# Optimization experiments

Hardware: AMD Instinct MI355X
Metric: run time of the kernel (lower is better)

## Reference

```python
import jax, jax.numpy as jnp
import numpy as np

B_, L_, D_ = 2, 4096, 1024
E_ = 2
DI = E_ * D_            # 2048
H_ = 16
HD_ = DI // H_          # 128
N_ = 128
K_ = 4                  # d_conv
CS_ = 256               # SSD chunk size
MC_ = 256               # Hebbian memory chunk size
ALPHA = 0.5             # memory_alpha (== write_alpha default)


def _silu(x):
    return x * jax.nn.sigmoid(x)


def _rmsnorm(x, w, eps=1e-6):
    return x * jax.lax.rsqrt(jnp.mean(x * x, axis=-1, keepdims=True) + eps) * w


def setup_inputs() -> dict:
    key = jax.random.key(0)
    ks = jax.random.split(key, 8)
    proj_dim = 2 * DI + 2 * H_ * N_ + H_
    n = lambda k, sh, sc: jax.random.normal(k, sh, jnp.float32) * sc
    return {
        "x": n(ks[0], (B_, L_, D_), 1.0),
        "norm_w": jnp.ones((D_,), jnp.float32),
        "w_in": n(ks[1], (proj_dim, D_), 0.02),
        "conv_w": n(ks[2], (DI, K_), 0.2),
        "conv_b": jnp.zeros((DI,), jnp.float32),
        "A_log": jnp.log(2.0 * jnp.ones((H_,), jnp.float32)),
        "dt_bias": jnp.zeros((H_,), jnp.float32),
        "D_skip": jnp.ones((DI,), jnp.float32),
        "w_out": n(ks[3], (D_, DI), 0.02),
        "w_write": n(ks[4], (D_, D_), 0.02),
        "w_read": n(ks[5], (D_, D_), 0.02),
        "decay": jnp.float32(4.6),
    }


def _forward(x, norm_w, w_in, conv_w, conv_b, A_log, dt_bias, D_skip,
             w_out, w_write, w_read, decay):
    B, L, D = x.shape
    residual = x
    xn = _rmsnorm(x, norm_w)

    # ---- SSDBlock ----
    proj = xn @ w_in.T  # (B,L,2*DI+2*H*N+H)
    val = proj[..., :DI]
    gate = proj[..., DI:2 * DI]
    Bp = proj[..., 2 * DI:2 * DI + H_ * N_].reshape(B, L, H_, N_)
    Cp = proj[..., 2 * DI + H_ * N_:2 * DI + 2 * H_ * N_].reshape(B, L, H_, N_)
    dt = jax.nn.softplus(proj[..., -H_:] + dt_bias)  # (B,L,H)

    # causal depthwise conv1d (kernel K_, groups=DI)
    vp = jnp.pad(val, ((0, 0), (K_ - 1, 0), (0, 0)))
    val = sum(conv_w[:, k] * vp[:, k:k + L, :] for k in range(K_)) + conv_b
    val = _silu(val).reshape(B, L, H_, HD_)

    ld = dt * (-jnp.exp(A_log))  # log decay (B,L,H)

    nc = L // CS_
    to_chunks = lambda a: jnp.moveaxis(a.reshape(B, nc, CS_, *a.shape[2:]), 1, 0)
    tril = jnp.tril(jnp.ones((CS_, CS_), bool))
    Dv = D_skip.reshape(1, H_, 1, HD_)

    def ssd_chunk(h, inp):
        v_c, b_c, c_c, ld_c = inp  # (B,CS,H,HD), (B,CS,H,N), (B,CS,H,N), (B,CS,H)
        cum = jnp.cumsum(ld_c, axis=1)            # (B,CS,H)
        cum_h = jnp.transpose(cum, (0, 2, 1))     # (B,H,CS)
        dd = cum_h[:, :, :, None] - cum_h[:, :, None, :]
        Lmat = jnp.where(tril, jnp.exp(dd), 0.0)
        M = jnp.einsum('blhn,bmhn->bhlm', c_c, b_c) * Lmat
        v_h = jnp.transpose(v_c, (0, 2, 1, 3))    # (B,H,CS,HD)
        Y = M @ v_h
        Y = Y + jnp.einsum('blhn,bhdn,blh->bhld', c_c, h, jnp.exp(cum))
        Y = Y + Dv * v_h
        h = jnp.exp(cum[:, -1])[:, :, None, None] * h + \
            jnp.einsum('blhd,blhn,blh->bhdn', v_c, b_c, jnp.exp(cum[:, -1:, :] - cum))
        return h, Y

    h0 = jnp.zeros((B, H_, HD_, N_), jnp.float32)
    _, Ys = jax.lax.scan(ssd_chunk, h0,
                         (to_chunks(val), to_chunks(Bp), to_chunks(Cp), to_chunks(ld)))
    # (nc,B,H,CS,HD) -> (B,L,DI)
    Y = jnp.transpose(Ys, (1, 0, 3, 2, 4)).reshape(B, L, DI)
    out = (Y * _silu(gate)) @ w_out.T  # (B,L,D)

    # ---- Hebbian memory (chunkwise) ----
    gamma = jax.nn.sigmoid(decay)
    lg = jnp.log(gamma)
    v = out @ w_write.T
    wk = jnp.pad(out[:, :-1], ((0, 0), (1, 0), (0, 0)))  # shifted write keys
    p = jnp.arange(MC_)
    diffs = jnp.maximum(p[:, None] - 1 - p[None, :], 0).astype(jnp.float32)
    causal = (p[:, None] > p[None, :]).astype(jnp.float32)
    Mmem = jnp.exp(diffs * lg) * causal
    gp = gamma ** p                    # read decay by position in chunk
    gw = gamma ** (MC_ - 1 - p)        # write decay to end of chunk
    nm = L // MC_
    tom = lambda a: jnp.moveaxis(a.reshape(B, nm, MC_, D), 1, 0)

    def mem_chunk(W, inp):
        rk_c, wk_c, v_c = inp  # (B,MC,D)
        inter = jnp.einsum('bde,bte->btd', W, rk_c) * gp[None, :, None]
        S = jnp.einsum('bie,bje->bij', rk_c, wk_c)
        intra = (S * Mmem) @ v_c
        W = gamma ** MC_ * W + jnp.einsum('btd,bte->bde', v_c * gw[None, :, None], wk_c)
        return W, inter + intra

    W0 = jnp.zeros((B, D, D), jnp.float32)
    _, reads = jax.lax.scan(mem_chunk, W0, (tom(out), tom(wk), tom(v)))
    reads = jnp.moveaxis(reads, 0, 1).reshape(B, L, D)
    out = out + ALPHA * (reads @ w_read.T)
    return residual + out


def reference(x, norm_w, w_in, conv_w, conv_b, A_log, dt_bias, D_skip,
              w_out, w_write, w_read, decay):
    return _forward(x, norm_w, w_in, conv_w, conv_b, A_log, dt_bias, D_skip,
                    w_out, w_write, w_read, decay)
```

## Files before the change

kernel.cpp:

```cpp
#include <hip/hip_runtime.h>
#include <hip/hip_bf16.h>

typedef __hip_bfloat16 bf16;
typedef __attribute__((ext_vector_type(8))) short short8;
typedef __attribute__((ext_vector_type(4))) float floatx4;

#define B_ 2
#define L_ 4096
#define D_ 1024
#define DI_ 2048
#define H_ 16
#define HD_ 128
#define N_ 128
#define CS_ 256
#define MC_ 256
#define NC_ 16
#define PROJ_ 8208

__device__ __forceinline__ float bf2f(short s) {
    return __uint_as_float(((unsigned)(unsigned short)s) << 16);
}

__device__ __forceinline__ void gl_lds16(const void* g, void* s) {
    __builtin_amdgcn_global_load_lds(
        (const __attribute__((address_space(1))) void*)g,
        (__attribute__((address_space(3))) void*)s, 16, 0, 0);
}

struct GemmP {
    const bf16* A; const bf16* Bt;
    float* C; bf16* CB; bf16* CB2; bf16* CB3;
    const float* add0; const float* add1; const bf16* add0b; const float* scr;
    long lda, ldb, ldc;
    int M, N, K, zinner;
    long a_zo, a_zi, b_zo, b_zi, c_zo, c_zi;
};

template<int EPI>
__global__ __launch_bounds__(256, 2) void gemm_bt(GemmP p)
{
    int NT = gridDim.x, MT = gridDim.y;
    long T = (long)NT * MT * gridDim.z;
    long flat = ((long)blockIdx.z * MT + blockIdx.y) * NT + blockIdx.x;
    int xcd = (int)(flat & 7);
    long q = flat >> 3;
    long Tq = T >> 3; int Tr = (int)(T & 7);
    long tile = (long)xcd * Tq + (long)(xcd < Tr ? xcd : Tr) + q;
    long per_z = (long)NT * MT;
    int z = (int)(tile / per_z);
    int t2 = (int)(tile - (long)z * per_z);
    int FG = NT >> 3;
    int g, width, within;
    if (t2 < FG * MT * 8) { g = t2 / (MT * 8); width = 8; within = t2 - g * MT * 8; }
    else                  { g = FG; width = NT - FG * 8; within = t2 - FG * MT * 8; }
    int m_outer = within / (8 * width);
    int hb = MT - m_outer * 8; if (hb > 8) hb = 8;
    int inner = within - m_outer * 8 * width;
    int n_in = inner / hb, m_in = inner - n_in * hb;
    int m0 = (m_outer * 8 + m_in) * 128;
    int n0 = (g * 8 + n_in) * 128;

    int zo = z / p.zinner, zi = z % p.zinner;
    const bf16* A  = p.A  + (long)zo * p.a_zo + (long)zi * p.a_zi;
    const bf16* Bt = p.Bt + (long)zo * p.b_zo + (long)zi * p.b_zi;
    long coff = (long)zo * p.c_zo + (long)zi * p.c_zi;

    __shared__ __align__(16) bf16 As[128 * 64];
    __shared__ __align__(16) bf16 Bs[128 * 64];

    int tid = threadIdx.x;
    int lane = tid & 63, wave = tid >> 6;
    int wm = (wave >> 1) * 64, wn = (wave & 1) * 64;
    int r16 = lane & 15, q8 = (lane >> 4) * 8;

    floatx4 zero4 = {0.f, 0.f, 0.f, 0.f};
    floatx4 acc[4][4];
#pragma unroll
    for (int i = 0; i < 4; i++)
#pragma unroll
        for (int j = 0; j < 4; j++) acc[i][j] = zero4;

    int lrow = lane >> 3;
    int lc = ((lane & 7) ^ lrow) * 8;
    int wrow = wave * 32;
    int rx = lane & 7;

    for (int k0 = 0; k0 < p.K; k0 += 64) {
#pragma unroll
        for (int t = 0; t < 4; t++) {
            int row = wrow + t * 8 + lrow;
            gl_lds16(A + (long)(m0 + row) * p.lda + k0 + lc, &As[(wrow + t * 8) * 64]);
            int bn = n0 + row; if (bn > p.N - 1) bn = p.N - 1;
            gl_lds16(Bt + (long)bn * p.ldb + k0 + lc, &Bs[(wrow + t * 8) * 64]);
        }
        __syncthreads();
#pragma unroll
        for (int ks = 0; ks < 64; ks += 32) {
            int lb = (ks >> 3) + (lane >> 4);
            int po = ((lb ^ rx) << 3);
            short8 af[4], bq[4];
#pragma unroll
            for (int i = 0; i < 4; i++)
                af[i] = *(const short8*)&As[(wm + i * 16 + r16) * 64 + po];
#pragma unroll
            for (int j = 0; j < 4; j++)
                bq[j] = *(const short8*)&Bs[(wn + j * 16 + r16) * 64 + po];
#pragma unroll
            for (int i = 0; i < 4; i++)
#pragma unroll
                for (int j = 0; j < 4; j++)
                    acc[i][j] = __builtin_amdgcn_mfma_f32_16x16x32_bf16(af[i], bq[j], acc[i][j], 0, 0, 0);
        }
        __syncthreads();
    }

    int rq = (lane >> 4) * 4;
#pragma unroll
    for (int i = 0; i < 4; i++) {
#pragma unroll
        for (int j = 0; j < 4; j++) {
#pragma unroll
            for (int r = 0; r < 4; r++) {
                int gm = m0 + wm + i * 16 + rq + r;
                int gn = n0 + wn + j * 16 + r16;
                if (gm >= p.M || gn >= p.N) continue;
                float a = acc[i][j][r];
                if (EPI == 0) {
                    p.C[coff + (long)gm * p.ldc + gn] = a;
                } else if (EPI == 1) {
                    long ix = coff + (long)gm * p.ldc + gn;
                    p.C[ix] = a; p.CB[ix] = __float2bfloat16(a);
                } else if (EPI == 2) {
                    if (gn < 2048)      p.CB [(long)gm * 2048 + gn]          = __float2bfloat16(a);
                    else if (gn < 4096) p.CB2[(long)gm * 2048 + (gn - 2048)] = __float2bfloat16(a);
                    else if (gn < 8192) p.CB3[(long)gm * 4096 + (gn - 4096)] = __float2bfloat16(a);
                    else                p.C  [(long)gm * 16   + (gn - 8192)] = a;
                } else if (EPI == 3) {
                    float lg = p.scr[1];
                    float v = (gm > gn) ? a * __expf((float)(gm - 1 - gn) * lg) : 0.f;
                    p.CB[coff + (long)gm * p.ldc + gn] = __float2bfloat16(v);
                } else if (EPI == 4) {
                    long ix = coff + (long)gm * p.ldc + gn;
                    float t = a * p.scr[16 + gm] + __bfloat162float(p.add0b[ix]);
                    p.CB[ix] = __float2bfloat16(t);
                } else if (EPI == 5) {
                    long ix = (long)gm * p.ldc + gn;
                    p.C[ix] = p.add0[ix] + p.add1[ix] + 0.5f * a;
                } else if (EPI == 6) {
                    p.CB[coff + (long)gm * p.ldc + gn] = __float2bfloat16(a);
                }
            }
        }
    }
}

__global__ void k_gamma(const float* decay, float* scr)
{
    int t = threadIdx.x;
    float g = 1.f / (1.f + expf(-decay[0]));
    float lg = logf(g);
    if (t == 0) { scr[0] = g; scr[1] = lg; scr[2] = expf(256.f * lg); }
    scr[16 + t]  = expf(lg * (float)t);
    scr[272 + t] = expf(lg * (float)(255 - t));
}

__global__ void k_f2b(const float* __restrict__ s, bf16* __restrict__ d, long n4)
{
    long i = (long)blockIdx.x * 256 + threadIdx.x;
    if (i >= n4) return;
    float4 v = ((const float4*)s)[i];
    bf16* o = d + i * 4;
    o[0] = __float2bfloat16(v.x); o[1] = __float2bfloat16(v.y);
    o[2] = __float2bfloat16(v.z); o[3] = __float2bfloat16(v.w);
}

__global__ __launch_bounds__(256) void k_rmsnorm(const float* __restrict__ x,
                                                 const float* __restrict__ w,
                                                 bf16* __restrict__ o)
{
    int row = blockIdx.x, t = threadIdx.x;
    float4 xv = ((const float4*)(x + (long)row * D_))[t];
    float s = xv.x*xv.x + xv.y*xv.y + xv.z*xv.z + xv.w*xv.w;
#pragma unroll
    for (int m = 32; m > 0; m >>= 1) s += __shfl_xor(s, m, 64);
    __shared__ float ps[4];
    if ((t & 63) == 0) ps[t >> 6] = s;
    __syncthreads();
    s = ps[0] + ps[1] + ps[2] + ps[3];
    float r = rsqrtf(s * (1.f / (float)D_) + 1e-6f);
    float4 wv = ((const float4*)w)[t];
    bf16* orow = o + (long)row * D_ + t * 4;
    orow[0] = __float2bfloat16(xv.x * r * wv.x);
    orow[1] = __float2bfloat16(xv.y * r * wv.y);
    orow[2] = __float2bfloat16(xv.z * r * wv.z);
    orow[3] = __float2bfloat16(xv.w * r * wv.w);
}

__global__ void k_ld(const float* __restrict__ dtr, const float* __restrict__ dt_bias,
                     const float* __restrict__ A_log, float* __restrict__ ld)
{
    long i = (long)blockIdx.x * 256 + threadIdx.x;
    if (i >= (long)B_ * L_ * H_) return;
    int h = (int)(i & 15);
    float d = dtr[i] + dt_bias[h];
    float sp = (d > 20.f) ? d : log1pf(__expf(d));
    ld[i] = -__expf(A_log[h]) * sp;
}

__global__ __launch_bounds__(256) void k_cum(const float* __restrict__ ld,
                                             float* __restrict__ cum_g,
                                             float* __restrict__ cumlast)
{
    int bid = blockIdx.x;
    int h = bid & 15, c = (bid >> 4) & 15, b = bid >> 8;
    long rowbase = (long)b * L_ + c * CS_;
    int tid = threadIdx.x;
    __shared__ float cum_s[256];
    cum_s[tid] = ld[(rowbase + tid) * H_ + h];
    __syncthreads();
    for (int off = 1; off < 256; off <<= 1) {
        float add = (tid >= off) ? cum_s[tid - off] : 0.f;
        __syncthreads();
        cum_s[tid] += add;
        __syncthreads();
    }
    cum_g[(rowbase + tid) * H_ + h] = cum_s[tid];
    if (tid == 255) cumlast[bid] = cum_s[255];
}

__global__ void k_conv(const bf16* __restrict__ val_b, const float* __restrict__ cw,
                       const float* __restrict__ cb, bf16* __restrict__ vo)
{
    long idx = (long)blockIdx.x * 256 + threadIdx.x;
    if (idx >= (long)B_ * L_ * DI_) return;
    long row = idx >> 11; int ch = (int)(idx & 2047);
    int l = (int)(row & (L_ - 1));
    float acc = cb[ch];
#pragma unroll
    for (int k = 0; k < 4; k++) {
        int ls = l - 3 + k;
        if (ls >= 0) acc += cw[ch * 4 + k] * __bfloat162float(val_b[(row - 3 + k) * 2048 + ch]);
    }
    float s = acc / (1.f + __expf(-acc));
    vo[idx] = __float2bfloat16(s);
}

__global__ void k_vt(const bf16* __restrict__ vconv, const float* __restrict__ cum_g,
                     const float* __restrict__ cumlast, bf16* __restrict__ vT,
                     bf16* __restrict__ vTw)
{
    __shared__ bf16 tile[32][33];
    int b = blockIdx.z;
    int r0 = blockIdx.x * 32, c0 = blockIdx.y * 32;
    int tx = threadIdx.x & 31, ty = threadIdx.x >> 5;
    for (int i = 0; i < 32; i += 8)
        tile[ty + i][tx] = vconv[((long)b * L_ + r0 + ty + i) * 2048 + c0 + tx];
    __syncthreads();
    int l = r0 + tx;
    int h = c0 >> 7;
    float w = __expf(cumlast[b * 256 + (l >> 8) * 16 + h] - cum_g[((long)b * L_ + l) * 16 + h]);
    for (int i = 0; i < 32; i += 8) {
        int col = c0 + ty + i;
        long oidx = ((long)b * 2048 + col) * L_ + l;
        bf16 v = tile[tx][ty + i];
        vT[oidx] = v;
        vTw[oidx] = __float2bfloat16(__bfloat162float(v) * w);
    }
}

__global__ void k_bt(const bf16* __restrict__ bc, bf16* __restrict__ BT)
{
    __shared__ bf16 tile[32][33];
    int b = blockIdx.z;
    int r0 = blockIdx.x * 32, c0 = blockIdx.y * 32;
    int tx = threadIdx.x & 31, ty = threadIdx.x >> 5;
    for (int i = 0; i < 32; i += 8)
        tile[ty + i][tx] = bc[((long)b * L_ + r0 + ty + i) * 4096 + c0 + tx];
    __syncthreads();
    int l = r0 + tx;
    for (int i = 0; i < 32; i += 8) {
        int col = c0 + ty + i;
        BT[((long)b * 2048 + col) * L_ + l] = tile[tx][ty + i];
    }
}

__global__ __launch_bounds__(256, 2) void k_ssd_u2(
    const bf16* __restrict__ vTw, const bf16* __restrict__ BT, float* __restrict__ U)
{
    int bid = blockIdx.x;
    int h = bid & 15, c = (bid >> 4) & 15, b = bid >> 8;
    int lane = threadIdx.x & 63, wave = threadIdx.x >> 6;
    int r16 = lane & 15, q8 = (lane >> 4) * 8, rq = (lane >> 4) * 4;
    int d0 = (wave >> 1) * 64, n0 = (wave & 1) * 64;
    const bf16* vb = vTw + ((long)b * 2048 + h * 128) * L_ + c * 256;
    const bf16* bb = BT  + ((long)b * 2048 + h * 128) * L_ + c * 256;
    floatx4 zero4 = {0.f, 0.f, 0.f, 0.f};
    floatx4 acc[4][4];
#pragma unroll
    for (int i = 0; i < 4; i++)
#pragma unroll
        for (int j = 0; j < 4; j++) acc[i][j] = zero4;
#pragma unroll 2
    for (int ks = 0; ks < 8; ks++) {
        short8 af[4], bq[4];
#pragma unroll
        for (int i = 0; i < 4; i++)
            af[i] = *(const short8*)(vb + (long)(d0 + i * 16 + r16) * L_ + ks * 32 + q8);
#pragma unroll
        for (int j = 0; j < 4; j++)
            bq[j] = *(const short8*)(bb + (long)(n0 + j * 16 + r16) * L_ + ks * 32 + q8);
#pragma unroll
        for (int i = 0; i < 4; i++)
#pragma unroll
            for (int j = 0; j < 4; j++)
                acc[i][j] = __builtin_amdgcn_mfma_f32_16x16x32_bf16(af[i], bq[j], acc[i][j], 0, 0, 0);
    }
    float* up = U + (((long)c * B_ + b) * H_ + h) * 16384;
#pragma unroll
    for (int i = 0; i < 4; i++)
#pragma unroll
        for (int j = 0; j < 4; j++)
#pragma unroll
            for (int r = 0; r < 4; r++)
                up[(d0 + i * 16 + rq + r) * 128 + (n0 + j * 16 + r16)] = acc[i][j][r];
}

__global__ void k_ssd2(const float* __restrict__ U, const float* __restrict__ cumlast,
                       bf16* __restrict__ hst)
{
    long idx = (long)blockIdx.x * 256 + threadIdx.x;
    const long tot = (long)B_ * H_ * HD_ * N_;
    if (idx >= tot) return;
    int bh = (int)(idx >> 14);
    int b = bh >> 4, h = bh & 15;
    float hv = 0.f;
    for (int c = 0; c < NC_; c++) {
        hst[c * tot + idx] = __float2bfloat16(hv);
        float ef = __expf(cumlast[b * 256 + c * 16 + h]);
        hv = ef * hv + U[c * tot + idx];
    }
}

__global__ __launch_bounds__(256, 2) void k_ssd_y(
    const bf16* __restrict__ bc_b, const bf16* __restrict__ vT,
    const bf16* __restrict__ hst, const float* __restrict__ cum_g,
    const float* __restrict__ Dskip, const bf16* __restrict__ gate_b,
    bf16* __restrict__ yg)
{
    int bid = blockIdx.x;
    int h = bid & 15, c = (bid >> 4) & 15, b = bid >> 8;
    long rowbase = (long)b * L_ + c * CS_;
    int tid = threadIdx.x, lane = tid & 63, wave = tid >> 6;
    int r16 = lane & 15, q8 = (lane >> 4) * 8, rq = (lane >> 4) * 4;
    int wt = (wave >> 1) * 32, wmS = (wave & 1) * 32, wd = (wave & 1) * 64;

    __shared__ float cum_s[256];
    __shared__ __align__(16) bf16 Ss[64][72];

    cum_s[tid] = cum_g[(rowbase + tid) * H_ + h];
    __syncthreads();

    const bf16* Cb  = bc_b + rowbase * 4096 + 2048 + h * 128;
    const bf16* Bb  = bc_b + rowbase * 4096 + h * 128;
    const bf16* vTb = vT + ((long)b * 2048 + h * 128) * L_ + c * 256;
    const bf16* hp  = hst + (((long)c * B_ + b) * H_ + h) * 16384;

    floatx4 zero4 = {0.f, 0.f, 0.f, 0.f};

    for (int tt = 0; tt < 4; tt++) {
        int tbase = tt * 64;
        short8 caf[2][4];
#pragma unroll
        for (int i = 0; i < 2; i++)
#pragma unroll
            for (int ks = 0; ks < 4; ks++)
                caf[i][ks] = *(const short8*)(Cb + (long)(tbase + wt + i * 16 + r16) * 4096 + ks * 32 + q8);

        floatx4 yacc[2][4];
#pragma unroll
        for (int i = 0; i < 2; i++)
#pragma unroll
            for (int j = 0; j < 4; j++) yacc[i][j] = zero4;
#pragma unroll
        for (int ks = 0; ks < 4; ks++)
#pragma unroll
            for (int j = 0; j < 4; j++) {
                short8 hq = *(const short8*)(hp + (long)(wd + j * 16 + r16) * 128 + ks * 32 + q8);
#pragma unroll
                for (int i = 0; i < 2; i++)
                    yacc[i][j] = __builtin_amdgcn_mfma_f32_16x16x32_bf16(caf[i][ks], hq, yacc[i][j], 0, 0, 0);
            }
        float texp[2][4];
#pragma unroll
        for (int i = 0; i < 2; i++)
#pragma unroll
            for (int r = 0; r < 4; r++)
                texp[i][r] = __expf(cum_s[tbase + wt + i * 16 + rq + r]);
#pragma unroll
        for (int i = 0; i < 2; i++)
#pragma unroll
            for (int j = 0; j < 4; j++)
#pragma unroll
                for (int r = 0; r < 4; r++) yacc[i][j][r] *= texp[i][r];

        for (int mt = 0; mt <= tt; mt++) {
            int mbase = mt * 64;
            floatx4 sacc[2][2];
#pragma unroll
            for (int i = 0; i < 2; i++)
#pragma unroll
                for (int j = 0; j < 2; j++) sacc[i][j] = zero4;
#pragma unroll
            for (int ks = 0; ks < 4; ks++) {
                short8 bq[2];
#pragma unroll
                for (int j = 0; j < 2; j++)
                    bq[j] = *(const short8*)(Bb + (long)(mbase + wmS + j * 16 + r16) * 4096 + ks * 32 + q8);
#pragma unroll
                for (int i = 0; i < 2; i++)
#pragma unroll
                    for (int j = 0; j < 2; j++)
                        sacc[i][j] = __builtin_amdgcn_mfma_f32_16x16x32_bf16(caf[i][ks], bq[j], sacc[i][j], 0, 0, 0);
            }
            __syncthreads();
#pragma unroll
            for (int i = 0; i < 2; i++)
#pragma unroll
                for (int r = 0; r < 4; r++) {
                    int trow = wt + i * 16 + rq + r;
                    float ct = cum_s[tbase + trow];
#pragma unroll
                    for (int j = 0; j < 2; j++) {
                        int mcol = mbase + wmS + j * 16 + r16;
                        float val = (mcol <= tbase + trow) ? sacc[i][j][r] * __expf(ct - cum_s[mcol]) : 0.f;
                        Ss[trow][wmS + j * 16 + r16] = __float2bfloat16(val);
                    }
                }
            __syncthreads();
#pragma unroll
            for (int ks = 0; ks < 2; ks++) {
                short8 saf[2];
#pragma unroll
                for (int i = 0; i < 2; i++)
                    saf[i] = *(const short8*)&Ss[wt + i * 16 + r16][ks * 32 + q8];
#pragma unroll
                for (int j = 0; j < 4; j++) {
                    short8 vq = *(const short8*)(vTb + (long)(wd + j * 16 + r16) * L_ + mbase + ks * 32 + q8);
#pragma unroll
                    for (int i = 0; i < 2; i++)
                        yacc[i][j] = __builtin_amdgcn_mfma_f32_16x16x32_bf16(saf[i], vq, yacc[i][j], 0, 0, 0);
                }
            }
        }
#pragma unroll
        for (int i = 0; i < 2; i++)
#pragma unroll
            for (int r = 0; r < 4; r++) {
                int t = tbase + wt + i * 16 + rq + r;
                long grow = (rowbase + t) * 2048 + h * 128;
#pragma unroll
                for (int j = 0; j < 4; j++) {
                    int d = wd + j * 16 + r16;
                    float vv = __bfloat162float(vTb[(long)d * L_ + t]);
                    float y = yacc[i][j][r] + Dskip[h * 128 + d] * vv;
                    float g = __bfloat162float(gate_b[grow + d]);
                    float sg = g / (1.f + __expf(-g));
                    yg[grow + d] = __float2bfloat16(y * sg);
                }
            }
    }
}

__global__ void k_shift(const bf16* __restrict__ ob, bf16* __restrict__ wk)
{
    long idx = (long)blockIdx.x * 256 + threadIdx.x;
    if (idx >= (long)B_ * L_ * D_) return;
    int l = (int)((idx >> 10) & (L_ - 1));
    wk[idx] = (l == 0) ? __float2bfloat16(0.f) : ob[idx - D_];
}

__global__ void k_transpose(const float* __restrict__ srcg, bf16* __restrict__ dstg)
{
    __shared__ float t[32][33];
    int b = blockIdx.z;
    const float* src = srcg + (long)b * L_ * D_;
    bf16* dst = dstg + (long)b * D_ * L_;
    int r0 = blockIdx.x * 32, c0 = blockIdx.y * 32;
    int tx = threadIdx.x & 31, ty = threadIdx.x >> 5;
    for (int i = 0; i < 32; i += 8)
        t[ty + i][tx] = src[(long)(r0 + ty + i) * D_ + c0 + tx];
    __syncthreads();
    for (int i = 0; i < 32; i += 8)
        dst[(long)(c0 + ty + i) * L_ + r0 + tx] = __float2bfloat16(t[tx][ty + i]);
}

__global__ void k_trans_wkg(const float* __restrict__ outg, const float* __restrict__ scr,
                            bf16* __restrict__ dstg)
{
    __shared__ float t[32][33];
    int b = blockIdx.z;
    const float* src = outg + (long)b * L_ * D_;
    bf16* dst = dstg + (long)b * D_ * L_;
    int r0 = blockIdx.x * 32, c0 = blockIdx.y * 32;
    int tx = threadIdx.x & 31, ty = threadIdx.x >> 5;
    for (int i = 0; i < 32; i += 8) {
        int rr = r0 + ty + i;
        float g = scr[272 + (rr & 255)];
        t[ty + i][tx] = (rr == 0) ? 0.f : src[(long)(rr - 1) * D_ + c0 + tx] * g;
    }
    __syncthreads();
    for (int i = 0; i < 32; i += 8)
        dst[(long)(c0 + ty + i) * L_ + r0 + tx] = __float2bfloat16(t[tx][ty + i]);
}

__global__ void k_m2(bf16* __restrict__ UwW, const float* __restrict__ scr)
{
    long idx = (long)blockIdx.x * 256 + threadIdx.x;
    const long tot = (long)B_ * D_ * D_;
    if (idx >= tot) return;
    float gMC = scr[2];
    float w = 0.f;
    for (int c = 0; c < NC_; c++) {
        float tmp = __bfloat162float(UwW[c * tot + idx]);
        UwW[c * tot + idx] = __float2bfloat16(w);
        w = gMC * w + tmp;
    }
}

static inline int cdiv_i(long a, long b) { return (int)((a + b - 1) / b); }

static void run_gemm(hipStream_t st, int epi, const bf16* A, const bf16* Bt,
                     float* C, bf16* CB, bf16* CB2, bf16* CB3,
                     const float* add0, const float* add1, const bf16* add0b,
                     const float* scr, int M, int N, int K,
                     long lda, long ldb, long ldc, int nbatch, int zinner,
                     long a_zo, long a_zi, long b_zo, long b_zi, long c_zo, long c_zi)
{
    GemmP p;
    p.A = A; p.Bt = Bt; p.C = C; p.CB = CB; p.CB2 = CB2; p.CB3 = CB3;
    p.add0 = add0; p.add1 = add1; p.add0b = add0b; p.scr = scr;
    p.lda = lda; p.ldb = ldb; p.ldc = ldc;
    p.M = M; p.N = N; p.K = K; p.zinner = zinner;
    p.a_zo = a_zo; p.a_zi = a_zi; p.b_zo = b_zo; p.b_zi = b_zi; p.c_zo = c_zo; p.c_zi = c_zi;
    dim3 g(cdiv_i(N, 128), cdiv_i(M, 128), nbatch);
    dim3 b(256);
    switch (epi) {
        case 0: gemm_bt<0><<<g, b, 0, st>>>(p); break;
        case 1: gemm_bt<1><<<g, b, 0, st>>>(p); break;
        case 2: gemm_bt<2><<<g, b, 0, st>>>(p); break;
        case 3: gemm_bt<3><<<g, b, 0, st>>>(p); break;
        case 4: gemm_bt<4><<<g, b, 0, st>>>(p); break;
        case 5: gemm_bt<5><<<g, b, 0, st>>>(p); break;
        case 6: gemm_bt<6><<<g, b, 0, st>>>(p); break;
    }
}

extern "C" void kernel_launch(void* const* d_in, const int* in_sizes, int n_in,
                              void* d_out, int out_size, void* d_ws, size_t ws_size,
                              hipStream_t stream)
{
    const float* x       = (const float*)d_in[0];
    const float* norm_w  = (const float*)d_in[1];
    const float* w_in    = (const float*)d_in[2];
    const float* conv_w  = (const float*)d_in[3];
    const float* conv_b  = (const float*)d_in[4];
    const float* A_log   = (const float*)d_in[5];
    const float* dt_bias = (const float*)d_in[6];
    const float* D_skip  = (const float*)d_in[7];
    const float* w_out   = (const float*)d_in[8];
    const float* w_write = (const float*)d_in[9];
    const float* w_read  = (const float*)d_in[10];
    const float* decay   = (const float*)d_in[11];
    float* outp = (float*)d_out;

    const size_t SZ_SCR  = 4096;
    const size_t SZ_DT   = (size_t)B_ * L_ * H_ * 4;
    const size_t SZ_CUML = 2048;
    const size_t SZ_WOUT = (size_t)D_ * DI_ * 2;
    const size_t SZ_WSML = (size_t)D_ * D_ * 2;
    const size_t SZ_R1   = (size_t)B_ * L_ * 2048 * 2;
    const size_t SZ_R2   = SZ_R1;
    const size_t SZ_R3   = (size_t)B_ * L_ * 4096 * 2;
    const size_t SZ_R4   = (size_t)B_ * L_ * D_ * 2 + (size_t)PROJ_ * D_ * 2;
    const size_t SZ_R5   = (size_t)B_ * L_ * 2048 * 4;

    size_t o = 0;
    auto take = [&](size_t sz) { size_t r = o; o += (sz + 255) & ~(size_t)255; return r; };
    const size_t O_SCR = take(SZ_SCR);
    const size_t O_DT  = take(SZ_DT);
    const size_t O_LD  = take(SZ_DT);
    const size_t O_CUM = take(SZ_DT);
    const size_t O_CL  = take(SZ_CUML);
    const size_t O_WO  = take(SZ_WOUT);
    const size_t O_WW  = take(SZ_WSML);
    const size_t O_WR  = take(SZ_WSML);
    const size_t O_R1  = take(SZ_R1);
    const size_t O_R2  = take(SZ_R2);
    const size_t O_R3  = take(SZ_R3);
    const size_t O_R4  = take(SZ_R4);
    const size_t O_R5  = take(SZ_R5);
    const size_t NEED = o;
    if (ws_size < NEED) return;

    char* ws = (char*)d_ws;
    float* scr     = (float*)(ws + O_SCR);
    float* dt_raw  = (float*)(ws + O_DT);
    float* ld_g    = (float*)(ws + O_LD);
    float* cum_g   = (float*)(ws + O_CUM);
    float* cumlast = (float*)(ws + O_CL);
    bf16*  w_out_b   = (bf16*)(ws + O_WO);
    bf16*  w_write_b = (bf16*)(ws + O_WW);
    bf16*  w_read_b  = (bf16*)(ws + O_WR);

    bf16*  val_b   = (bf16*)(ws + O_R1);
    bf16*  vTw_g   = (bf16*)(ws + O_R1);
    bf16*  yg_b    = (bf16*)(ws + O_R1);
    bf16*  hst_b   = (bf16*)(ws + O_R1 + (size_t)B_ * L_ * D_ * 2);
    bf16*  Sm_b    = (bf16*)(ws + O_R1);
    bf16*  intra_b = (bf16*)(ws + O_R1 + (size_t)NC_ * B_ * MC_ * MC_ * 2);
    bf16*  gate_b  = (bf16*)(ws + O_R2);
    bf16*  out_b   = (bf16*)(ws + O_R2);
    bf16*  wk_b    = (bf16*)(ws + O_R2 + (size_t)B_ * L_ * D_ * 2);
    bf16*  reads_b = wk_b;
    bf16*  bc_b    = (bf16*)(ws + O_R3);
    bf16*  UwW     = (bf16*)(ws + O_R3);
    bf16*  xn_b    = (bf16*)(ws + O_R4);
    bf16*  w_in_b  = (bf16*)(ws + O_R4 + (size_t)B_ * L_ * D_ * 2);
    bf16*  vconv_b = (bf16*)(ws + O_R4);
    float* U_ssd   = (float*)(ws + O_R4);
    float* outf    = (float*)(ws + O_R4);
    bf16*  vT_g    = (bf16*)(ws + O_R5);
    bf16*  BT_g    = (bf16*)(ws + O_R5 + (size_t)B_ * L_ * 2048 * 2);
    float* vbuf    = (float*)(ws + O_R5);
    bf16*  vTm     = (bf16*)(ws + O_R5 + (size_t)B_ * L_ * D_ * 4);
    bf16*  wkgT    = (bf16*)(ws + O_R5 + (size_t)B_ * L_ * D_ * 4 + (size_t)B_ * L_ * D_ * 2);

    const long BLD  = (long)B_ * L_ * D_;
    const long BLDI = (long)B_ * L_ * DI_;

    k_gamma<<<1, 256, 0, stream>>>(decay, scr);
    k_f2b<<<cdiv_i((long)PROJ_ * D_ / 4, 256), 256, 0, stream>>>(w_in, w_in_b, (long)PROJ_ * D_ / 4);
    k_f2b<<<cdiv_i((long)D_ * DI_ / 4, 256), 256, 0, stream>>>(w_out, w_out_b, (long)D_ * DI_ / 4);
    k_f2b<<<cdiv_i((long)D_ * D_ / 4, 256), 256, 0, stream>>>(w_write, w_write_b, (long)D_ * D_ / 4);
    k_f2b<<<cdiv_i((long)D_ * D_ / 4, 256), 256, 0, stream>>>(w_read, w_read_b, (long)D_ * D_ / 4);
    k_rmsnorm<<<B_ * L_, 256, 0, stream>>>(x, norm_w, xn_b);
    run_gemm(stream, 2, xn_b, w_in_b, dt_raw, val_b, gate_b, bc_b, nullptr, nullptr, nullptr, nullptr,
             B_ * L_, PROJ_, D_, D_, D_, 0, 1, 1, 0, 0, 0, 0, 0, 0);
    k_ld<<<cdiv_i((long)B_ * L_ * H_, 256), 256, 0, stream>>>(dt_raw, dt_bias, A_log, ld_g);
    k_cum<<<B_ * NC_ * H_, 256, 0, stream>>>(ld_g, cum_g, cumlast);
    k_conv<<<cdiv_i(BLDI, 256), 256, 0, stream>>>(val_b, conv_w, conv_b, vconv_b);
    k_vt<<<dim3(L_ / 32, DI_ / 32, B_), 256, 0, stream>>>(vconv_b, cum_g, cumlast, vT_g, vTw_g);
    k_bt<<<dim3(L_ / 32, DI_ / 32, B_), 256, 0, stream>>>(bc_b, BT_g);
    k_ssd_u2<<<B_ * NC_ * H_, 256, 0, stream>>>(vTw_g, BT_g, U_ssd);
    k_ssd2<<<cdiv_i((long)B_ * H_ * HD_ * N_, 256), 256, 0, stream>>>(U_ssd, cumlast, hst_b);
    k_ssd_y<<<B_ * NC_ * H_, 256, 0, stream>>>(bc_b, vT_g, hst_b, cum_g, D_skip, gate_b, yg_b);
    run_gemm(stream, 1, yg_b, w_out_b, outf, out_b, nullptr, nullptr, nullptr, nullptr, nullptr, nullptr,
             B_ * L_, D_, DI_, DI_, DI_, D_, 1, 1, 0, 0, 0, 0, 0, 0);
    k_shift<<<cdiv_i(BLD, 256), 256, 0, stream>>>(out_b, wk_b);
    run_gemm(stream, 0, out_b, w_write_b, vbuf, nullptr, nullptr, nullptr, nullptr, nullptr, nullptr, nullptr,
             B_ * L_, D_, D_, D_, D_, D_, 1, 1, 0, 0, 0, 0, 0, 0);
    k_transpose<<<dim3(L_ / 32, D_ / 32, B_), 256, 0, stream>>>(vbuf, vTm);
    k_trans_wkg<<<dim3(L_ / 32, D_ / 32, B_), 256, 0, stream>>>(outf, scr, wkgT);
    run_gemm(stream, 6, vTm, wkgT, nullptr, UwW, nullptr, nullptr, nullptr, nullptr, nullptr, nullptr,
             D_, D_, MC_, L_, L_, D_, B_ * NC_, NC_,
             (long)D_ * L_, MC_, (long)D_ * L_, MC_, (long)D_ * D_, (long)B_ * D_ * D_);
    k_m2<<<cdiv_i((long)B_ * D_ * D_, 256), 256, 0, stream>>>(UwW, scr);
    run_gemm(stream, 3, out_b, wk_b, nullptr, Sm_b, nullptr, nullptr, nullptr, nullptr, nullptr, scr,
             MC_, MC_, D_, D_, D_, MC_, B_ * NC_, NC_,
             (long)L_ * D_, (long)MC_ * D_, (long)L_ * D_, (long)MC_ * D_,
             (long)MC_ * MC_, (long)B_ * MC_ * MC_);
    run_gemm(stream, 6, Sm_b, vTm, nullptr, intra_b, nullptr, nullptr, nullptr, nullptr, nullptr, nullptr,
             MC_, D_, MC_, MC_, L_, D_, B_ * NC_, NC_,
             (long)MC_ * MC_, (long)B_ * MC_ * MC_, (long)D_ * L_, MC_,
             (long)L_ * D_, (long)MC_ * D_);
    run_gemm(stream, 4, out_b, UwW, nullptr, reads_b, nullptr, nullptr, nullptr, nullptr, intra_b, scr,
             MC_, D_, D_, D_, D_, D_, B_ * NC_, NC_,
             (long)L_ * D_, (long)MC_ * D_, (long)D_ * D_, (long)B_ * D_ * D_,
             (long)L_ * D_, (long)MC_ * D_);
    run_gemm(stream, 5, reads_b, w_read_b, outp, nullptr, nullptr, nullptr, x, outf, nullptr, nullptr,
             B_ * L_, D_, D_, D_, D_, D_, 1, 1, 0, 0, 0, 0, 0, 0);
}
```

Measured before the change: 824.3 us.

## Fuse small elementwise kernels and drop fp32 intermediates in the SSD pipeline

Merges the four weight-conversion launches into one kernel and folds the log-decay computation into the cumulative-sum kernel. The depthwise conv is fused into the transpose, and the per-position decay weighting moves into the SSD state GEMM's operand load. The out-projection and write GEMMs now emit only bf16, and the final GEMM reads the bf16 residual. This removes launches and fp32 round-trips through memory, at the cost of using bf16 rather than fp32 for the out-projection term added in the final epilogue.

```diff
diff --git a/kernel.cpp b/kernel.cpp
--- a/kernel.cpp
+++ b/kernel.cpp
@@ -127,9 +127,6 @@
                 float a = acc[i][j][r];
                 if (EPI == 0) {
                     p.C[coff + (long)gm * p.ldc + gn] = a;
-                } else if (EPI == 1) {
-                    long ix = coff + (long)gm * p.ldc + gn;
-                    p.C[ix] = a; p.CB[ix] = __float2bfloat16(a);
                 } else if (EPI == 2) {
                     if (gn < 2048)      p.CB [(long)gm * 2048 + gn]          = __float2bfloat16(a);
                     else if (gn < 4096) p.CB2[(long)gm * 2048 + (gn - 2048)] = __float2bfloat16(a);
@@ -143,11 +140,11 @@
                     long ix = coff + (long)gm * p.ldc + gn;
                     float t = a * p.scr[16 + gm] + __bfloat162float(p.add0b[ix]);
                     p.CB[ix] = __float2bfloat16(t);
-                } else if (EPI == 5) {
-                    long ix = (long)gm * p.ldc + gn;
-                    p.C[ix] = p.add0[ix] + p.add1[ix] + 0.5f * a;
                 } else if (EPI == 6) {
                     p.CB[coff + (long)gm * p.ldc + gn] = __float2bfloat16(a);
+                } else if (EPI == 7) {
+                    long ix = (long)gm * p.ldc + gn;
+                    p.C[ix] = p.add0[ix] + __bfloat162float(p.add0b[ix]) + 0.5f * a;
                 }
             }
         }
@@ -164,12 +161,23 @@
     scr[272 + t] = expf(lg * (float)(255 - t));
 }
 
-__global__ void k_f2b(const float* __restrict__ s, bf16* __restrict__ d, long n4)
+__global__ void k_f2ball(const float* __restrict__ s0, bf16* __restrict__ d0, long n0,
+                         const float* __restrict__ s1, bf16* __restrict__ d1, long n1,
+                         const float* __restrict__ s2, bf16* __restrict__ d2, long n2,
+                         const float* __restrict__ s3, bf16* __restrict__ d3, long n3)
 {
     long i = (long)blockIdx.x * 256 + threadIdx.x;
-    if (i >= n4) return;
-    float4 v = ((const float4*)s)[i];
-    bf16* o = d + i * 4;
+    const float* s; bf16* d; long rel = i;
+    if (rel < n0) { s = s0; d = d0; }
+    else { rel -= n0;
+        if (rel < n1) { s = s1; d = d1; }
+        else { rel -= n1;
+            if (rel < n2) { s = s2; d = d2; }
+            else { rel -= n2; if (rel >= n3) return; s = s3; d = d3; }
+        }
+    }
+    float4 v = ((const float4*)s)[rel];
+    bf16* o = d + rel * 4;
     o[0] = __float2bfloat16(v.x); o[1] = __float2bfloat16(v.y);
     o[2] = __float2bfloat16(v.z); o[3] = __float2bfloat16(v.w);
 }
@@ -196,18 +204,9 @@
     orow[3] = __float2bfloat16(xv.w * r * wv.w);
 }
 
-__global__ void k_ld(const float* __restrict__ dtr, const float* __restrict__ dt_bias,
-                     const float* __restrict__ A_log, float* __restrict__ ld)
-{
-    long i = (long)blockIdx.x * 256 + threadIdx.x;
-    if (i >= (long)B_ * L_ * H_) return;
-    int h = (int)(i & 15);
-    float d = dtr[i] + dt_bias[h];
-    float sp = (d > 20.f) ? d : log1pf(__expf(d));
-    ld[i] = -__expf(A_log[h]) * sp;
-}
-
-__global__ __launch_bounds__(256) void k_cum(const float* __restrict__ ld,
+__global__ __launch_bounds__(256) void k_cum(const float* __restrict__ dtr,
+                                             const float* __restrict__ dt_bias,
+                                             const float* __restrict__ A_log,
                                              float* __restrict__ cum_g,
                                              float* __restrict__ cumlast)
 {
@@ -216,7 +215,9 @@
     long rowbase = (long)b * L_ + c * CS_;
     int tid = threadIdx.x;
     __shared__ float cum_s[256];
-    cum_s[tid] = ld[(rowbase + tid) * H_ + h];
+    float d = dtr[(rowbase + tid) * H_ + h] + dt_bias[h];
+    float sp = (d > 20.f) ? d : log1pf(__expf(d));
+    cum_s[tid] = -__expf(A_log[h]) * sp;
     __syncthreads();
     for (int off = 1; off < 256; off <<= 1) {
         float add = (tid >= off) ? cum_s[tid - off] : 0.f;
@@ -228,43 +229,33 @@
     if (tid == 255) cumlast[bid] = cum_s[255];
 }
 
-__global__ void k_conv(const bf16* __restrict__ val_b, const float* __restrict__ cw,
-                       const float* __restrict__ cb, bf16* __restrict__ vo)
-{
-    long idx = (long)blockIdx.x * 256 + threadIdx.x;
-    if (idx >= (long)B_ * L_ * DI_) return;
-    long row = idx >> 11; int ch = (int)(idx & 2047);
-    int l = (int)(row & (L_ - 1));
-    float acc = cb[ch];
-#pragma unroll
-    for (int k = 0; k < 4; k++) {
-        int ls = l - 3 + k;
-        if (ls >= 0) acc += cw[ch * 4 + k] * __bfloat162float(val_b[(row - 3 + k) * 2048 + ch]);
-    }
-    float s = acc / (1.f + __expf(-acc));
-    vo[idx] = __float2bfloat16(s);
-}
-
-__global__ void k_vt(const bf16* __restrict__ vconv, const float* __restrict__ cum_g,
-                     const float* __restrict__ cumlast, bf16* __restrict__ vT,
-                     bf16* __restrict__ vTw)
-{
-    __shared__ bf16 tile[32][33];
+__global__ void k_vtc(const bf16* __restrict__ val_b, const float* __restrict__ cw,
+                      const float* __restrict__ cb, bf16* __restrict__ vT)
+{
+    __shared__ bf16 tile[35][33];
     int b = blockIdx.z;
     int r0 = blockIdx.x * 32, c0 = blockIdx.y * 32;
-    int tx = threadIdx.x & 31, ty = threadIdx.x >> 5;
-    for (int i = 0; i < 32; i += 8)
-        tile[ty + i][tx] = vconv[((long)b * L_ + r0 + ty + i) * 2048 + c0 + tx];
-    __syncthreads();
+    int tid = threadIdx.x;
+    for (int idx = tid; idx < 35 * 32; idx += 256) {
+        int row = idx >> 5, ch = idx & 31;
+        int gl = r0 - 3 + row;
+        bf16 v = __float2bfloat16(0.f);
+        if (gl >= 0 && gl < L_) v = val_b[((long)b * L_ + gl) * 2048 + c0 + ch];
+        tile[row][ch] = v;
+    }
+    __syncthreads();
+    int tx = tid & 31, ty = tid >> 5;
     int l = r0 + tx;
-    int h = c0 >> 7;
-    float w = __expf(cumlast[b * 256 + (l >> 8) * 16 + h] - cum_g[((long)b * L_ + l) * 16 + h]);
     for (int i = 0; i < 32; i += 8) {
-        int col = c0 + ty + i;
-        long oidx = ((long)b * 2048 + col) * L_ + l;
-        bf16 v = tile[tx][ty + i];
-        vT[oidx] = v;
-        vTw[oidx] = __float2bfloat16(__bfloat162float(v) * w);
+        int ch = c0 + ty + i;
+        float4 cwv = ((const float4*)cw)[ch];
+        float acc = cb[ch]
+                  + cwv.x * __bfloat162float(tile[tx][ty + i])
+                  + cwv.y * __bfloat162float(tile[tx + 1][ty + i])
+                  + cwv.z * __bfloat162float(tile[tx + 2][ty + i])
+                  + cwv.w * __bfloat162float(tile[tx + 3][ty + i]);
+        float s = acc / (1.f + __expf(-acc));
+        vT[((long)b * 2048 + ch) * L_ + l] = __float2bfloat16(s);
     }
 }
 
@@ -285,15 +276,22 @@
 }
 
 __global__ __launch_bounds__(256, 2) void k_ssd_u2(
-    const bf16* __restrict__ vTw, const bf16* __restrict__ BT, float* __restrict__ U)
+    const bf16* __restrict__ vT, const bf16* __restrict__ BT,
+    const float* __restrict__ cum_g, const float* __restrict__ cumlast,
+    float* __restrict__ U)
 {
     int bid = blockIdx.x;
     int h = bid & 15, c = (bid >> 4) & 15, b = bid >> 8;
-    int lane = threadIdx.x & 63, wave = threadIdx.x >> 6;
+    long rowbase = (long)b * L_ + c * CS_;
+    int tid = threadIdx.x;
+    __shared__ float w_s[256];
+    w_s[tid] = __expf(cumlast[bid] - cum_g[(rowbase + tid) * H_ + h]);
+    __syncthreads();
+    int lane = tid & 63, wave = tid >> 6;
     int r16 = lane & 15, q8 = (lane >> 4) * 8, rq = (lane >> 4) * 4;
     int d0 = (wave >> 1) * 64, n0 = (wave & 1) * 64;
-    const bf16* vb = vTw + ((long)b * 2048 + h * 128) * L_ + c * 256;
-    const bf16* bb = BT  + ((long)b * 2048 + h * 128) * L_ + c * 256;
+    const bf16* vb = vT + ((long)b * 2048 + h * 128) * L_ + c * 256;
+    const bf16* bb = BT + ((long)b * 2048 + h * 128) * L_ + c * 256;
     floatx4 zero4 = {0.f, 0.f, 0.f, 0.f};
     floatx4 acc[4][4];
 #pragma unroll
@@ -302,10 +300,20 @@
         for (int j = 0; j < 4; j++) acc[i][j] = zero4;
 #pragma unroll 2
     for (int ks = 0; ks < 8; ks++) {
+        float wv[8];
+#pragma unroll
+        for (int j = 0; j < 8; j++) wv[j] = w_s[ks * 32 + q8 + j];
         short8 af[4], bq[4];
 #pragma unroll
-        for (int i = 0; i < 4; i++)
-            af[i] = *(const short8*)(vb + (long)(d0 + i * 16 + r16) * L_ + ks * 32 + q8);
+        for (int i = 0; i < 4; i++) {
+            short8 raw = *(const short8*)(vb + (long)(d0 + i * 16 + r16) * L_ + ks * 32 + q8);
+#pragma unroll
+            for (int j = 0; j < 8; j++) {
+                float f = bf2f(raw[j]) * wv[j];
+                raw[j] = (short)(__float_as_uint(f) >> 16);
+            }
+            af[i] = raw;
+        }
 #pragma unroll
         for (int j = 0; j < 4; j++)
             bq[j] = *(const short8*)(bb + (long)(n0 + j * 16 + r16) * L_ + ks * 32 + q8);
@@ -479,11 +487,11 @@
     wk[idx] = (l == 0) ? __float2bfloat16(0.f) : ob[idx - D_];
 }
 
-__global__ void k_transpose(const float* __restrict__ srcg, bf16* __restrict__ dstg)
-{
-    __shared__ float t[32][33];
+__global__ void k_transpose_b(const bf16* __restrict__ srcg, bf16* __restrict__ dstg)
+{
+    __shared__ bf16 t[32][33];
     int b = blockIdx.z;
-    const float* src = srcg + (long)b * L_ * D_;
+    const bf16* src = srcg + (long)b * L_ * D_;
     bf16* dst = dstg + (long)b * D_ * L_;
     int r0 = blockIdx.x * 32, c0 = blockIdx.y * 32;
     int tx = threadIdx.x & 31, ty = threadIdx.x >> 5;
@@ -491,22 +499,22 @@
         t[ty + i][tx] = src[(long)(r0 + ty + i) * D_ + c0 + tx];
     __syncthreads();
     for (int i = 0; i < 32; i += 8)
-        dst[(long)(c0 + ty + i) * L_ + r0 + tx] = __float2bfloat16(t[tx][ty + i]);
-}
-
-__global__ void k_trans_wkg(const float* __restrict__ outg, const float* __restrict__ scr,
+        dst[(long)(c0 + ty + i) * L_ + r0 + tx] = t[tx][ty + i];
+}
+
+__global__ void k_trans_wkg(const bf16* __restrict__ outg, const float* __restrict__ scr,
                             bf16* __restrict__ dstg)
 {
     __shared__ float t[32][33];
     int b = blockIdx.z;
-    const float* src = outg + (long)b * L_ * D_;
+    const bf16* src = outg + (long)b * L_ * D_;
     bf16* dst = dstg + (long)b * D_ * L_;
     int r0 = blockIdx.x * 32, c0 = blockIdx.y * 32;
     int tx = threadIdx.x & 31, ty = threadIdx.x >> 5;
     for (int i = 0; i < 32; i += 8) {
         int rr = r0 + ty + i;
         float g = scr[272 + (rr & 255)];
-        t[ty + i][tx] = (rr == 0) ? 0.f : src[(long)(rr - 1) * D_ + c0 + tx] * g;
+        t[ty + i][tx] = (rr == 0) ? 0.f : __bfloat162float(src[(long)(rr - 1) * D_ + c0 + tx]) * g;
     }
     __syncthreads();
     for (int i = 0; i < 32; i += 8)
@@ -546,12 +554,11 @@
     dim3 b(256);
     switch (epi) {
         case 0: gemm_bt<0><<<g, b, 0, st>>>(p); break;
-        case 1: gemm_bt<1><<<g, b, 0, st>>>(p); break;
         case 2: gemm_bt<2><<<g, b, 0, st>>>(p); break;
         case 3: gemm_bt<3><<<g, b, 0, st>>>(p); break;
         case 4: gemm_bt<4><<<g, b, 0, st>>>(p); break;
-        case 5: gemm_bt<5><<<g, b, 0, st>>>(p); break;
         case 6: gemm_bt<6><<<g, b, 0, st>>>(p); break;
+        case 7: gemm_bt<7><<<g, b, 0, st>>>(p); break;
     }
 }
 
@@ -601,11 +608,11 @@
     const size_t O_R5  = take(SZ_R5);
     const size_t NEED = o;
     if (ws_size < NEED) return;
+    (void)O_LD;
 
     char* ws = (char*)d_ws;
     float* scr     = (float*)(ws + O_SCR);
     float* dt_raw  = (float*)(ws + O_DT);
-    float* ld_g    = (float*)(ws + O_LD);
     float* cum_g   = (float*)(ws + O_CUM);
     float* cumlast = (float*)(ws + O_CL);
     bf16*  w_out_b   = (bf16*)(ws + O_WO);
@@ -613,7 +620,6 @@
     bf16*  w_read_b  = (bf16*)(ws + O_WR);
 
     bf16*  val_b   = (bf16*)(ws + O_R1);
-    bf16*  vTw_g   = (bf16*)(ws + O_R1);
     bf16*  yg_b    = (bf16*)(ws + O_R1);
     bf16*  hst_b   = (bf16*)(ws + O_R1 + (size_t)B_ * L_ * D_ * 2);
     bf16*  Sm_b    = (bf16*)(ws + O_R1);
@@ -626,41 +632,38 @@
     bf16*  UwW     = (bf16*)(ws + O_R3);
     bf16*  xn_b    = (bf16*)(ws + O_R4);
     bf16*  w_in_b  = (bf16*)(ws + O_R4 + (size_t)B_ * L_ * D_ * 2);
-    bf16*  vconv_b = (bf16*)(ws + O_R4);
     float* U_ssd   = (float*)(ws + O_R4);
-    float* outf    = (float*)(ws + O_R4);
     bf16*  vT_g    = (bf16*)(ws + O_R5);
     bf16*  BT_g    = (bf16*)(ws + O_R5 + (size_t)B_ * L_ * 2048 * 2);
-    float* vbuf    = (float*)(ws + O_R5);
+    bf16*  vbuf_b  = (bf16*)(ws + O_R5);
     bf16*  vTm     = (bf16*)(ws + O_R5 + (size_t)B_ * L_ * D_ * 4);
     bf16*  wkgT    = (bf16*)(ws + O_R5 + (size_t)B_ * L_ * D_ * 4 + (size_t)B_ * L_ * D_ * 2);
 
-    const long BLD  = (long)B_ * L_ * D_;
-    const long BLDI = (long)B_ * L_ * DI_;
+    const long BLD = (long)B_ * L_ * D_;
 
     k_gamma<<<1, 256, 0, stream>>>(decay, scr);
-    k_f2b<<<cdiv_i((long)PROJ_ * D_ / 4, 256), 256, 0, stream>>>(w_in, w_in_b, (long)PROJ_ * D_ / 4);
-    k_f2b<<<cdiv_i((long)D_ * DI_ / 4, 256), 256, 0, stream>>>(w_out, w_out_b, (long)D_ * DI_ / 4);
-    k_f2b<<<cdiv_i((long)D_ * D_ / 4, 256), 256, 0, stream>>>(w_write, w_write_b, (long)D_ * D_ / 4);
-    k_f2b<<<cdiv_i((long)D_ * D_ / 4, 256), 256, 0, stream>>>(w_read, w_read_b, (long)D_ * D_ / 4);
+    {
+        long n0 = (long)PROJ_ * D_ / 4, n1 = (long)D_ * DI_ / 4;
+        long n2 = (long)D_ * D_ / 4,   n3 = n2;
+        k_f2ball<<<cdiv_i(n0 + n1 + n2 + n3, 256), 256, 0, stream>>>(
+            w_in, w_in_b, n0, w_out, w_out_b, n1, w_write, w_write_b, n2, w_read, w_read_b, n3);
+    }
     k_rmsnorm<<<B_ * L_, 256, 0, stream>>>(x, norm_w, xn_b);
     run_gemm(stream, 2, xn_b, w_in_b, dt_raw, val_b, gate_b, bc_b, nullptr, nullptr, nullptr, nullptr,
              B_ * L_, PROJ_, D_, D_, D_, 0, 1, 1, 0, 0, 0, 0, 0, 0);
-    k_ld<<<cdiv_i((long)B_ * L_ * H_, 256), 256, 0, stream>>>(dt_raw, dt_bias, A_log, ld_g);
-    k_cum<<<B_ * NC_ * H_, 256, 0, stream>>>(ld_g, cum_g, cumlast);
-    k_conv<<<cdiv_i(BLDI, 256), 256, 0, stream>>>(val_b, conv_w, conv_b, vconv_b);
-    k_vt<<<dim3(L_ / 32, DI_ / 32, B_), 256, 0, stream>>>(vconv_b, cum_g, cumlast, vT_g, vTw_g);
+    k_cum<<<B_ * NC_ * H_, 256, 0, stream>>>(dt_raw, dt_bias, A_log, cum_g, cumlast);
+    k_vtc<<<dim3(L_ / 32, DI_ / 32, B_), 256, 0, stream>>>(val_b, conv_w, conv_b, vT_g);
     k_bt<<<dim3(L_ / 32, DI_ / 32, B_), 256, 0, stream>>>(bc_b, BT_g);
-    k_ssd_u2<<<B_ * NC_ * H_, 256, 0, stream>>>(vTw_g, BT_g, U_ssd);
+    k_ssd_u2<<<B_ * NC_ * H_, 256, 0, stream>>>(vT_g, BT_g, cum_g, cumlast, U_ssd);
     k_ssd2<<<cdiv_i((long)B_ * H_ * HD_ * N_, 256), 256, 0, stream>>>(U_ssd, cumlast, hst_b);
     k_ssd_y<<<B_ * NC_ * H_, 256, 0, stream>>>(bc_b, vT_g, hst_b, cum_g, D_skip, gate_b, yg_b);
-    run_gemm(stream, 1, yg_b, w_out_b, outf, out_b, nullptr, nullptr, nullptr, nullptr, nullptr, nullptr,
+    run_gemm(stream, 6, yg_b, w_out_b, nullptr, out_b, nullptr, nullptr, nullptr, nullptr, nullptr, nullptr,
              B_ * L_, D_, DI_, DI_, DI_, D_, 1, 1, 0, 0, 0, 0, 0, 0);
     k_shift<<<cdiv_i(BLD, 256), 256, 0, stream>>>(out_b, wk_b);
-    run_gemm(stream, 0, out_b, w_write_b, vbuf, nullptr, nullptr, nullptr, nullptr, nullptr, nullptr, nullptr,
+    run_gemm(stream, 6, out_b, w_write_b, nullptr, vbuf_b, nullptr, nullptr, nullptr, nullptr, nullptr, nullptr,
              B_ * L_, D_, D_, D_, D_, D_, 1, 1, 0, 0, 0, 0, 0, 0);
-    k_transpose<<<dim3(L_ / 32, D_ / 32, B_), 256, 0, stream>>>(vbuf, vTm);
-    k_trans_wkg<<<dim3(L_ / 32, D_ / 32, B_), 256, 0, stream>>>(outf, scr, wkgT);
+    k_transpose_b<<<dim3(L_ / 32, D_ / 32, B_), 256, 0, stream>>>(vbuf_b, vTm);
+    k_trans_wkg<<<dim3(L_ / 32, D_ / 32, B_), 256, 0, stream>>>(out_b, scr, wkgT);
     run_gemm(stream, 6, vTm, wkgT, nullptr, UwW, nullptr, nullptr, nullptr, nullptr, nullptr, nullptr,
              D_, D_, MC_, L_, L_, D_, B_ * NC_, NC_,
              (long)D_ * L_, MC_, (long)D_ * L_, MC_, (long)D_ * D_, (long)B_ * D_ * D_);
@@ -677,6 +680,6 @@
              MC_, D_, D_, D_, D_, D_, B_ * NC_, NC_,
              (long)L_ * D_, (long)MC_ * D_, (long)D_ * D_, (long)B_ * D_ * D_,
              (long)L_ * D_, (long)MC_ * D_);
-    run_gemm(stream, 5, reads_b, w_read_b, outp, nullptr, nullptr, nullptr, x, outf, nullptr, nullptr,
+    run_gemm(stream, 7, reads_b, w_read_b, outp, nullptr, nullptr, nullptr, x, nullptr, out_b, nullptr,
              B_ * L_, D_, D_, D_, D_, D_, 1, 1, 0, 0, 0, 0, 0, 0);
 }
```

New measurement: 813.5 us. No clear change (-1.3%).
